# Optimization experiments

Measured on AMD Instinct MI355X. Metric: run time of the kernel, lower is better.

## Reference

```python
import jax, jax.numpy as jnp
import numpy as np

EMBED_DIM = 1024
NUM_HEADS = 16
DIM_K = EMBED_DIM // NUM_HEADS
B, S = 2, 2048


def setup_inputs() -> dict:
    key = jax.random.key(0)
    ks = jax.random.split(key, 7)
    scale = 1.0 / np.sqrt(EMBED_DIM)
    return {
        "query": jax.random.normal(ks[0], (B, S, EMBED_DIM), dtype=jnp.float32),
        "key": jax.random.normal(ks[1], (B, S, EMBED_DIM), dtype=jnp.float32),
        "value": jax.random.normal(ks[2], (B, S, EMBED_DIM), dtype=jnp.float32),
        "Wq": jax.random.normal(ks[3], (EMBED_DIM, EMBED_DIM), dtype=jnp.float32) * scale,
        "Wk": jax.random.normal(ks[4], (EMBED_DIM, EMBED_DIM), dtype=jnp.float32) * scale,
        "Wv": jax.random.normal(ks[5], (EMBED_DIM, EMBED_DIM), dtype=jnp.float32) * scale,
        "Wo": jax.random.normal(ks[6], (EMBED_DIM, EMBED_DIM), dtype=jnp.float32) * scale,
    }


def reference(query, key, value, Wq, Wk, Wv, Wo):
    b, s, e = query.shape
    # nn.Linear: y = x @ W.T  (bias=False)
    def proj(x, W):
        y = x @ W.T  # [b, s, e]
        return y.reshape(b, -1, NUM_HEADS, DIM_K).transpose(0, 2, 1, 3)  # [b, h, s, dk]

    q = proj(query, Wq)
    k = proj(key, Wk)
    v = proj(value, Wv)

    # attention: scores = q k^T / sqrt(dk); softmax; @ v  (dropout p=0 in eval)
    scores = jnp.einsum("bhqd,bhkd->bhqk", q, k) / jnp.sqrt(jnp.float32(DIM_K))
    attn = jax.nn.softmax(scores, axis=-1)
    x = jnp.einsum("bhqk,bhkd->bhqd", attn, v)  # [b, h, s, dk]

    x = x.transpose(0, 2, 1, 3).reshape(b, -1, e)  # merge heads
    return x @ Wo.T
```

## Files before the change

kernel.cpp:

```cpp
#include <hip/hip_runtime.h>
#include <hip/hip_bf16.h>
#include <stdint.h>

#define EMBED 1024
#define NHEAD 16
#define DKD   64
#define BATCH 2
#define SEQ   2048
#define MROWS (BATCH*SEQ)

typedef __attribute__((ext_vector_type(8)))  short bf16x8;
typedef __attribute__((ext_vector_type(4)))  float f32x4;
typedef __attribute__((ext_vector_type(16))) float f32x16;
typedef unsigned short u16;
typedef unsigned int   u32;
typedef __attribute__((ext_vector_type(4))) u32 u32x4;

__device__ inline u16 f2bf(float f) {
  return __builtin_bit_cast(u16, __float2bfloat16(f));
}

__device__ inline u32 cvtpk(float lo, float hi) {
  u32 r;
  asm("v_cvt_pk_bf16_f32 %0, %1, %2" : "=v"(r) : "v"(lo), "v"(hi));
  return r;
}

__device__ inline void plswap(u32& x, u32& y) {
  asm volatile("v_permlane32_swap_b32 %0, %1" : "+v"(x), "+v"(y));
}

__device__ inline void gload_lds16(const u16* g, u16* l) {
  __builtin_amdgcn_global_load_lds(
      (const __attribute__((address_space(1))) u32*)(const void*)g,
      (__attribute__((address_space(3))) u32*)(void*)l, 16, 0, 0);
}

__global__ __launch_bounds__(256) void cast_all(
    const float* __restrict__ s0, const float* __restrict__ s1,
    const float* __restrict__ s2, const float* __restrict__ s3,
    const float* __restrict__ s4, const float* __restrict__ s5,
    const float* __restrict__ s6,
    u16* __restrict__ d0, u16* __restrict__ d1, u16* __restrict__ d2,
    u16* __restrict__ d3, u16* __restrict__ d4, u16* __restrict__ d5,
    u16* __restrict__ d6) {
  const int y = blockIdx.y;
  const float* s; u16* d; int n4;
  switch (y) {
    case 0: s = s0; d = d0; n4 = MROWS*EMBED/4; break;
    case 1: s = s1; d = d1; n4 = MROWS*EMBED/4; break;
    case 2: s = s2; d = d2; n4 = MROWS*EMBED/4; break;
    case 3: s = s3; d = d3; n4 = EMBED*EMBED/4; break;
    case 4: s = s4; d = d4; n4 = EMBED*EMBED/4; break;
    case 5: s = s5; d = d5; n4 = EMBED*EMBED/4; break;
    default: s = s6; d = d6; n4 = EMBED*EMBED/4; break;
  }
  int i = blockIdx.x * 256 + threadIdx.x;
  int stride = gridDim.x * 256;
  for (int idx = i; idx < n4; idx += stride) {
    float4 f = ((const float4*)s)[idx];
    ushort4 o;
    o.x = f2bf(f.x); o.y = f2bf(f.y); o.z = f2bf(f.z); o.w = f2bf(f.w);
    ((ushort4*)d)[idx] = o;
  }
}

__global__ __launch_bounds__(256)
void gemm_qkv(const u16* __restrict__ A0, const u16* __restrict__ A1,
              const u16* __restrict__ A2, const u16* __restrict__ B0,
              const u16* __restrict__ B1, const u16* __restrict__ B2,
              u16* __restrict__ C0, u16* __restrict__ C1, u16* __restrict__ C2) {
  constexpr int K = EMBED;
  __shared__ u16 As[128 * 32];
  __shared__ u16 Bs[128 * 32];
  const int z = blockIdx.z;
  const u16* A = (z == 0) ? A0 : (z == 1) ? A1 : A2;
  const u16* B = (z == 0) ? B0 : (z == 1) ? B1 : B2;
  u16* C       = (z == 0) ? C0 : (z == 1) ? C1 : C2;

  const int t = threadIdx.x;
  const int w = t >> 6, l = t & 63;
  const int lr = l & 15, lg = l >> 4;
  const int m0 = blockIdx.x * 128;
  const int n0 = blockIdx.y * 128;
  const int wr = (w >> 1) * 64, wc = (w & 1) * 64;

  f32x4 acc[4][4] = {};

  const int srow = t >> 2;
  const int scol = (t & 3) * 8;
  const u16* Ag = A + (size_t)(m0 + srow) * K + scol;
  const u16* Bg = B + (size_t)(n0 + srow) * K + scol;
  u16* AsW = As + w * 512;
  u16* BsW = Bs + w * 512;
  const size_t rowstep = (size_t)64 * K;

  for (int k0 = 0; k0 < K; k0 += 32) {
    gload_lds16(Ag + k0,           AsW);
    gload_lds16(Ag + k0 + rowstep, AsW + 64 * 32);
    gload_lds16(Bg + k0,           BsW);
    gload_lds16(Bg + k0 + rowstep, BsW + 64 * 32);
    __syncthreads();
    bf16x8 a[4], b[4];
#pragma unroll
    for (int r = 0; r < 4; r++)
      a[r] = *(const bf16x8*)(As + (wr + r * 16 + lr) * 32 + 8 * lg);
#pragma unroll
    for (int c = 0; c < 4; c++)
      b[c] = *(const bf16x8*)(Bs + (wc + c * 16 + lr) * 32 + 8 * lg);
#pragma unroll
    for (int r = 0; r < 4; r++)
#pragma unroll
      for (int c = 0; c < 4; c++)
        acc[r][c] = __builtin_amdgcn_mfma_f32_16x16x32_bf16(a[r], b[c], acc[r][c], 0, 0, 0);
    __syncthreads();
  }

#pragma unroll
  for (int r = 0; r < 4; r++)
#pragma unroll
    for (int c = 0; c < 4; c++)
#pragma unroll
      for (int j = 0; j < 4; j++) {
        int m = m0 + wr + r * 16 + lg * 4 + j;
        int n = n0 + wc + c * 16 + lr;
        int b_ = m >> 11, s_ = m & 2047;
        int h_ = n >> 6,  d_ = n & 63;
        u16 vv = f2bf(acc[r][c][j]);
        if (z == 2)
          C[((size_t)(b_ * NHEAD + h_) * DKD + d_) * SEQ + s_] = vv;
        else
          C[(((size_t)(b_ * NHEAD + h_) * SEQ + s_) << 6) + d_] = vv;
      }
}

__global__ __launch_bounds__(256)
void gemm_out(const u16* __restrict__ A, const u16* __restrict__ B,
              float* __restrict__ C) {
  constexpr int K = EMBED, N = EMBED;
  __shared__ u16 As[64 * 32];
  __shared__ u16 Bs[128 * 32];
  const int t = threadIdx.x;
  const int w = t >> 6, l = t & 63;
  const int lr = l & 15, lg = l >> 4;
  const int m0 = blockIdx.x * 64;
  const int n0 = blockIdx.y * 128;
  const int wr = (w >> 1) * 32, wc = (w & 1) * 64;

  f32x4 acc[2][4] = {};

  const int srow = t >> 2;
  const int scol = (t & 3) * 8;
  const u16* Ag = A + (size_t)(m0 + srow) * K + scol;
  const u16* Bg = B + (size_t)(n0 + srow) * K + scol;
  u16* AsW = As + w * 512;
  u16* BsW = Bs + w * 512;
  const size_t rowstep = (size_t)64 * K;

  for (int k0 = 0; k0 < K; k0 += 32) {
    gload_lds16(Ag + k0,           AsW);
    gload_lds16(Bg + k0,           BsW);
    gload_lds16(Bg + k0 + rowstep, BsW + 64 * 32);
    __syncthreads();
    bf16x8 a[2], b[4];
#pragma unroll
    for (int r = 0; r < 2; r++)
      a[r] = *(const bf16x8*)(As + (wr + r * 16 + lr) * 32 + 8 * lg);
#pragma unroll
    for (int c = 0; c < 4; c++)
      b[c] = *(const bf16x8*)(Bs + (wc + c * 16 + lr) * 32 + 8 * lg);
#pragma unroll
    for (int r = 0; r < 2; r++)
#pragma unroll
      for (int c = 0; c < 4; c++)
        acc[r][c] = __builtin_amdgcn_mfma_f32_16x16x32_bf16(a[r], b[c], acc[r][c], 0, 0, 0);
    __syncthreads();
  }

#pragma unroll
  for (int r = 0; r < 2; r++)
#pragma unroll
    for (int c = 0; c < 4; c++)
#pragma unroll
      for (int j = 0; j < 4; j++) {
        int m = m0 + wr + r * 16 + lg * 4 + j;
        int n = n0 + wc + c * 16 + lr;
        C[(size_t)m * N + n] = acc[r][c][j];
      }
}

__global__ __launch_bounds__(256, 2)
void attn_kernel(const u16* __restrict__ Qh, const u16* __restrict__ Kh,
                 const u16* __restrict__ Vt, u16* __restrict__ Xo) {
  __shared__ u16 KV[2][8192];
  const int t = threadIdx.x, w = t >> 6, l = t & 63;
  const int q32 = l & 31, h = l >> 5;
  const int xcd = blockIdx.x & 7;
  const int li  = blockIdx.x >> 3;
  const int bh  = xcd * 4 + (li >> 4);
  const int qblk = li & 15;
  const int b_ = bh >> 4, h_ = bh & 15;
  const size_t base = (size_t)bh * SEQ * DKD;
  const u16* Kb = Kh + base;
  const u16* Vb = Vt + base;
  constexpr int NT = SEQ / 64;
  constexpr float C2 = 0.18033688f;
  constexpr float THR = 44.0f;

  const int qrow = qblk * 128 + w * 32 + q32;
  bf16x8 qf[4];
#pragma unroll
  for (int ks = 0; ks < 4; ks++)
    qf[ks] = *(const bf16x8*)(Qh + base + (size_t)qrow * DKD + ks * 16 + h * 8);

  f32x16 acc[2] = {};
  float m2 = -1e30f, lsum = 0.f;

  auto stage = [&](int buf, int kt) {
    u16* kd = &KV[buf][0];
    u16* vd = &KV[buf][4096];
    const int rb = w * 8 + (l >> 3);
    const int sg = (l & 7) ^ (l >> 3);
#pragma unroll
    for (int ch = 0; ch < 2; ch++) {
      int row = ch * 32 + rb;
      gload_lds16(Kb + (size_t)(kt * 64 + row) * DKD + sg * 8,
                  kd + (ch * 32 + w * 8) * 64);
      gload_lds16(Vb + (size_t)row * SEQ + kt * 64 + sg * 8,
                  vd + (ch * 32 + w * 8) * 64);
    }
  };

  auto compute = [&](int buf) {
    const u16* kd = &KV[buf][0];
    const u16* vd = &KV[buf][4096];
    f32x16 s[2] = {};
#pragma unroll
    for (int c = 0; c < 2; c++) {
      int row = c * 32 + q32;
#pragma unroll
      for (int ks = 0; ks < 4; ks++) {
        bf16x8 kf = *(const bf16x8*)(kd + row * 64 + (((2 * ks + h) ^ (row & 7)) * 8));
        s[c] = __builtin_amdgcn_mfma_f32_32x32x16_bf16(kf, qf[ks], s[c], 0, 0, 0);
      }
    }
    bf16x8 vf[2][4];
#pragma unroll
    for (int dc = 0; dc < 2; dc++) {
      int row = dc * 32 + q32;
#pragma unroll
      for (int tile = 0; tile < 4; tile++)
        vf[dc][tile] = *(const bf16x8*)(vd + row * 64 + (((2 * tile + h) ^ (row & 7)) * 8));
    }
    float pm = s[0][0];
#pragma unroll
    for (int r = 1; r < 16; r++) pm = fmaxf(pm, s[0][r]);
#pragma unroll
    for (int r = 0; r < 16; r++) pm = fmaxf(pm, s[1][r]);
    if (__any(pm > m2 + THR)) {
      float pmo = __shfl_xor(pm, 32, 64);
      float mn = fmaxf(m2, fmaxf(pm, pmo));
      float al = __builtin_amdgcn_exp2f((m2 - mn) * C2);
      lsum *= al;
#pragma unroll
      for (int dc = 0; dc < 2; dc++)
#pragma unroll
        for (int r = 0; r < 16; r++) acc[dc][r] *= al;
      m2 = mn;
    }
    const float nm = -m2 * C2;
    bf16x8 pfrag[4];
    float ls = 0.f;
#pragma unroll
    for (int c = 0; c < 2; c++) {
      float p[16];
#pragma unroll
      for (int r = 0; r < 16; r++) {
        p[r] = __builtin_amdgcn_exp2f(__builtin_fmaf(s[c][r], C2, nm));
        ls += p[r];
      }
      u32 Pk[8];
#pragma unroll
      for (int i = 0; i < 8; i++) Pk[i] = cvtpk(p[2 * i], p[2 * i + 1]);
      plswap(Pk[0], Pk[2]); plswap(Pk[1], Pk[3]);
      plswap(Pk[4], Pk[6]); plswap(Pk[5], Pk[7]);
      pfrag[2 * c]     = __builtin_bit_cast(bf16x8, (u32x4){Pk[0], Pk[1], Pk[2], Pk[3]});
      pfrag[2 * c + 1] = __builtin_bit_cast(bf16x8, (u32x4){Pk[4], Pk[5], Pk[6], Pk[7]});
    }
    lsum += ls;
#pragma unroll
    for (int tile = 0; tile < 4; tile++)
#pragma unroll
      for (int dc = 0; dc < 2; dc++)
        acc[dc] = __builtin_amdgcn_mfma_f32_32x32x16_bf16(vf[dc][tile], pfrag[tile], acc[dc], 0, 0, 0);
  };

  stage(0, 0);
  __syncthreads();
  int cur = 0;
  for (int kt = 0; kt < NT; kt++) {
    if (kt + 1 < NT) stage(cur ^ 1, kt + 1);
    compute(cur);
    __syncthreads();
    cur ^= 1;
  }

  lsum += __shfl_xor(lsum, 32, 64);
  float inv = 1.0f / lsum;
  u16* orow = Xo + ((size_t)b_ * SEQ + qrow) * EMBED + h_ * DKD;
#pragma unroll
  for (int dc = 0; dc < 2; dc++)
#pragma unroll
    for (int k4 = 0; k4 < 4; k4++) {
      u32 w0 = cvtpk(acc[dc][4 * k4 + 0] * inv, acc[dc][4 * k4 + 1] * inv);
      u32 w1 = cvtpk(acc[dc][4 * k4 + 2] * inv, acc[dc][4 * k4 + 3] * inv);
      int d = dc * 32 + k4 * 8 + h * 4;
      uint2 pk; pk.x = w0; pk.y = w1;
      *(uint2*)(orow + d) = pk;
    }
}

extern "C" void kernel_launch(void* const* d_in, const int* in_sizes, int n_in,
                              void* d_out, int out_size, void* d_ws, size_t ws_size,
                              hipStream_t stream) {
  const float* q  = (const float*)d_in[0];
  const float* k  = (const float*)d_in[1];
  const float* v  = (const float*)d_in[2];
  const float* Wq = (const float*)d_in[3];
  const float* Wk = (const float*)d_in[4];
  const float* Wv = (const float*)d_in[5];
  const float* Wo = (const float*)d_in[6];

  char* ws = (char*)d_ws;
  const size_t SZ_X = (size_t)MROWS * EMBED * 2;
  const size_t SZ_W = (size_t)EMBED * EMBED * 2;
  u16* qbf  = (u16*)(ws);
  u16* kbf  = (u16*)(ws + SZ_X);
  u16* vbf  = (u16*)(ws + 2 * SZ_X);
  u16* wqb  = (u16*)(ws + 3 * SZ_X);
  u16* wkb  = (u16*)(ws + 3 * SZ_X + SZ_W);
  u16* wvb  = (u16*)(ws + 3 * SZ_X + 2 * SZ_W);
  u16* wob  = (u16*)(ws + 3 * SZ_X + 3 * SZ_W);
  u16* Qh   = (u16*)(ws + 3 * SZ_X + 4 * SZ_W);
  u16* Kh   = (u16*)(ws + 4 * SZ_X + 4 * SZ_W);
  u16* Vt   = (u16*)(ws + 5 * SZ_X + 4 * SZ_W);
  u16* Xcat = (u16*)(ws + 6 * SZ_X + 4 * SZ_W);

  cast_all<<<dim3(1024, 7), 256, 0, stream>>>(q, k, v, Wq, Wk, Wv, Wo,
                                              qbf, kbf, vbf, wqb, wkb, wvb, wob);

  gemm_qkv<<<dim3(MROWS / 128, EMBED / 128, 3), 256, 0, stream>>>(
      qbf, kbf, vbf, wqb, wkb, wvb, Qh, Kh, Vt);

  attn_kernel<<<512, 256, 0, stream>>>(Qh, Kh, Vt, Xcat);

  gemm_out<<<dim3(MROWS / 64, EMBED / 128), 256, 0, stream>>>(Xcat, wob, (float*)d_out);
}
```

Before: 122.4 us.

## Split attention KV range across two wave groups and merge partial softmax

Doubles the attention block to 512 threads; two groups of four waves each process half the key sequence for the same 128 query rows with separate LDS double buffers. After the loop, the second half's partial accumulators, max and sum are written to LDS and merged by the first half with rescaling before output. It also changes the LDS swizzle to include the chunk and wave index, and turns the row-max and row-sum reductions into trees for more ILP. The aim is more waves per CU and shorter serial KV loops to hide latency, in exchange for higher LDS use, an extra merge step and fewer blocks resident per CU.

```diff
diff --git a/kernel.cpp b/kernel.cpp
--- a/kernel.cpp
+++ b/kernel.cpp
@@ -189,12 +189,13 @@
       }
 }
 
-__global__ __launch_bounds__(256, 2)
+__global__ __launch_bounds__(512, 4)
 void attn_kernel(const u16* __restrict__ Qh, const u16* __restrict__ Kh,
                  const u16* __restrict__ Vt, u16* __restrict__ Xo) {
-  __shared__ u16 KV[2][8192];
+  __shared__ u16 KV[2][2][8192];
   const int t = threadIdx.x, w = t >> 6, l = t & 63;
   const int q32 = l & 31, h = l >> 5;
+  const int hv = w >> 2, wq = w & 3;
   const int xcd = blockIdx.x & 7;
   const int li  = blockIdx.x >> 3;
   const int bh  = xcd * 4 + (li >> 4);
@@ -203,11 +204,11 @@
   const size_t base = (size_t)bh * SEQ * DKD;
   const u16* Kb = Kh + base;
   const u16* Vb = Vt + base;
-  constexpr int NT = SEQ / 64;
+  constexpr int NT2 = SEQ / 64 / 2;
   constexpr float C2 = 0.18033688f;
   constexpr float THR = 44.0f;
 
-  const int qrow = qblk * 128 + w * 32 + q32;
+  const int qrow = qblk * 128 + wq * 32 + q32;
   bf16x8 qf[4];
 #pragma unroll
   for (int ks = 0; ks < 4; ks++)
@@ -217,30 +218,32 @@
   float m2 = -1e30f, lsum = 0.f;
 
   auto stage = [&](int buf, int kt) {
-    u16* kd = &KV[buf][0];
-    u16* vd = &KV[buf][4096];
-    const int rb = w * 8 + (l >> 3);
-    const int sg = (l & 7) ^ (l >> 3);
+    u16* kd = &KV[hv][buf][0];
+    u16* vd = &KV[hv][buf][4096];
+    const int rb = wq * 8 + (l >> 3);
+    const int ktile = hv * NT2 + kt;
 #pragma unroll
     for (int ch = 0; ch < 2; ch++) {
       int row = ch * 32 + rb;
-      gload_lds16(Kb + (size_t)(kt * 64 + row) * DKD + sg * 8,
-                  kd + (ch * 32 + w * 8) * 64);
-      gload_lds16(Vb + (size_t)row * SEQ + kt * 64 + sg * 8,
-                  vd + (ch * 32 + w * 8) * 64);
+      int sg = (l & 7) ^ (l >> 3) ^ (ch * 4 + wq);
+      gload_lds16(Kb + (size_t)(ktile * 64 + row) * DKD + sg * 8,
+                  kd + (ch * 32 + wq * 8) * 64);
+      gload_lds16(Vb + (size_t)row * SEQ + ktile * 64 + sg * 8,
+                  vd + (ch * 32 + wq * 8) * 64);
     }
   };
 
   auto compute = [&](int buf) {
-    const u16* kd = &KV[buf][0];
-    const u16* vd = &KV[buf][4096];
+    const u16* kd = &KV[hv][buf][0];
+    const u16* vd = &KV[hv][buf][4096];
     f32x16 s[2] = {};
 #pragma unroll
     for (int c = 0; c < 2; c++) {
       int row = c * 32 + q32;
+      int key = (q32 & 7) ^ (c * 4 + (q32 >> 3));
 #pragma unroll
       for (int ks = 0; ks < 4; ks++) {
-        bf16x8 kf = *(const bf16x8*)(kd + row * 64 + (((2 * ks + h) ^ (row & 7)) * 8));
+        bf16x8 kf = *(const bf16x8*)(kd + row * 64 + (((2 * ks + h) ^ key) * 8));
         s[c] = __builtin_amdgcn_mfma_f32_32x32x16_bf16(kf, qf[ks], s[c], 0, 0, 0);
       }
     }
@@ -248,15 +251,19 @@
 #pragma unroll
     for (int dc = 0; dc < 2; dc++) {
       int row = dc * 32 + q32;
+      int key = (q32 & 7) ^ (dc * 4 + (q32 >> 3));
 #pragma unroll
       for (int tile = 0; tile < 4; tile++)
-        vf[dc][tile] = *(const bf16x8*)(vd + row * 64 + (((2 * tile + h) ^ (row & 7)) * 8));
-    }
-    float pm = s[0][0];
-#pragma unroll
-    for (int r = 1; r < 16; r++) pm = fmaxf(pm, s[0][r]);
-#pragma unroll
-    for (int r = 0; r < 16; r++) pm = fmaxf(pm, s[1][r]);
+        vf[dc][tile] = *(const bf16x8*)(vd + row * 64 + (((2 * tile + h) ^ key) * 8));
+    }
+    float mx[16];
+#pragma unroll
+    for (int r = 0; r < 16; r++) mx[r] = fmaxf(s[0][r], s[1][r]);
+#pragma unroll
+    for (int off = 8; off >= 1; off >>= 1)
+#pragma unroll
+      for (int r = 0; r < off; r++) mx[r] = fmaxf(mx[r], mx[r + off]);
+    float pm = mx[0];
     if (__any(pm > m2 + THR)) {
       float pmo = __shfl_xor(pm, 32, 64);
       float mn = fmaxf(m2, fmaxf(pm, pmo));
@@ -275,10 +282,11 @@
     for (int c = 0; c < 2; c++) {
       float p[16];
 #pragma unroll
-      for (int r = 0; r < 16; r++) {
+      for (int r = 0; r < 16; r++)
         p[r] = __builtin_amdgcn_exp2f(__builtin_fmaf(s[c][r], C2, nm));
-        ls += p[r];
-      }
+      float s0 = ((p[0] + p[1]) + (p[2] + p[3])) + ((p[4] + p[5]) + (p[6] + p[7]));
+      float s1 = ((p[8] + p[9]) + (p[10] + p[11])) + ((p[12] + p[13]) + (p[14] + p[15]));
+      ls += s0 + s1;
       u32 Pk[8];
 #pragma unroll
       for (int i = 0; i < 8; i++) Pk[i] = cvtpk(p[2 * i], p[2 * i + 1]);
@@ -298,26 +306,51 @@
   stage(0, 0);
   __syncthreads();
   int cur = 0;
-  for (int kt = 0; kt < NT; kt++) {
-    if (kt + 1 < NT) stage(cur ^ 1, kt + 1);
+  for (int kt = 0; kt < NT2; kt++) {
+    if (kt + 1 < NT2) stage(cur ^ 1, kt + 1);
     compute(cur);
     __syncthreads();
     cur ^= 1;
   }
 
-  lsum += __shfl_xor(lsum, 32, 64);
-  float inv = 1.0f / lsum;
-  u16* orow = Xo + ((size_t)b_ * SEQ + qrow) * EMBED + h_ * DKD;
-#pragma unroll
-  for (int dc = 0; dc < 2; dc++)
-#pragma unroll
-    for (int k4 = 0; k4 < 4; k4++) {
-      u32 w0 = cvtpk(acc[dc][4 * k4 + 0] * inv, acc[dc][4 * k4 + 1] * inv);
-      u32 w1 = cvtpk(acc[dc][4 * k4 + 2] * inv, acc[dc][4 * k4 + 3] * inv);
-      int d = dc * 32 + k4 * 8 + h * 4;
-      uint2 pk; pk.x = w0; pk.y = w1;
-      *(uint2*)(orow + d) = pk;
-    }
+  float* shf = (float*)&KV[0][0][0];
+  if (hv == 1) {
+    float* dst = shf + (size_t)(wq * 64 + l) * 36;
+#pragma unroll
+    for (int dc = 0; dc < 2; dc++)
+#pragma unroll
+      for (int k4 = 0; k4 < 4; k4++) {
+        float4 v4o = {acc[dc][4 * k4 + 0], acc[dc][4 * k4 + 1],
+                      acc[dc][4 * k4 + 2], acc[dc][4 * k4 + 3]};
+        *(float4*)(dst + dc * 16 + k4 * 4) = v4o;
+      }
+    dst[32] = m2;
+    dst[33] = lsum;
+  }
+  __syncthreads();
+  if (hv == 0) {
+    const float* src = shf + (size_t)(wq * 64 + l) * 36;
+    float m2b = src[32], lsb = src[33];
+    float mN = fmaxf(m2, m2b);
+    float a0 = __builtin_amdgcn_exp2f((m2 - mN) * C2);
+    float a1 = __builtin_amdgcn_exp2f((m2b - mN) * C2);
+    float lv = lsum * a0 + lsb * a1;
+    lv += __shfl_xor(lv, 32, 64);
+    float inv = 1.0f / lv;
+    u16* orow = Xo + ((size_t)b_ * SEQ + qrow) * EMBED + h_ * DKD;
+#pragma unroll
+    for (int dc = 0; dc < 2; dc++)
+#pragma unroll
+      for (int k4 = 0; k4 < 4; k4++) {
+        float4 ob = *(const float4*)(src + dc * 16 + k4 * 4);
+        float o0 = (acc[dc][4 * k4 + 0] * a0 + ob.x * a1) * inv;
+        float o1 = (acc[dc][4 * k4 + 1] * a0 + ob.y * a1) * inv;
+        float o2 = (acc[dc][4 * k4 + 2] * a0 + ob.z * a1) * inv;
+        float o3 = (acc[dc][4 * k4 + 3] * a0 + ob.w * a1) * inv;
+        uint2 pk; pk.x = cvtpk(o0, o1); pk.y = cvtpk(o2, o3);
+        *(uint2*)(orow + dc * 32 + k4 * 8 + h * 4) = pk;
+      }
+  }
 }
 
 extern "C" void kernel_launch(void* const* d_in, const int* in_sizes, int n_in,
@@ -352,7 +385,7 @@
   gemm_qkv<<<dim3(MROWS / 128, EMBED / 128, 3), 256, 0, stream>>>(
       qbf, kbf, vbf, wqb, wkb, wvb, Qh, Kh, Vt);
 
-  attn_kernel<<<512, 256, 0, stream>>>(Qh, Kh, Vt, Xcat);
+  attn_kernel<<<512, 512, 0, stream>>>(Qh, Kh, Vt, Xcat);
 
   gemm_out<<<dim3(MROWS / 64, EMBED / 128), 256, 0, stream>>>(Xcat, wob, (float*)d_out);
 }
```

New measurement: 146.8 us. 20.0% more time.

## Split attention over key halves with a separate log-sum-exp combine kernel

Applied to the files above, without the earlier changes.

Splits the attention key sequence into two halves, doubling the grid to 1024 blocks. Each block writes partial normalized outputs plus per-row max and sum, and a new combine kernel merges the two halves with log-sum-exp weights. Launch bounds are raised to four blocks per SM. The goal is better occupancy and CU fill on the MI355X's many CUs for the 512-block attention. The cost is an extra kernel launch, extra global traffic for the partials, and an extra bf16 rounding of the partial outputs.

```diff
diff --git a/kernel.cpp b/kernel.cpp
--- a/kernel.cpp
+++ b/kernel.cpp
@@ -18,6 +18,10 @@
 
 __device__ inline u16 f2bf(float f) {
   return __builtin_bit_cast(u16, __float2bfloat16(f));
+}
+__device__ inline float bf2f(u16 x) {
+  u32 u = ((u32)x) << 16;
+  return __builtin_bit_cast(float, u);
 }
 
 __device__ inline u32 cvtpk(float lo, float hi) {
@@ -189,9 +193,10 @@
       }
 }
 
-__global__ __launch_bounds__(256, 2)
-void attn_kernel(const u16* __restrict__ Qh, const u16* __restrict__ Kh,
-                 const u16* __restrict__ Vt, u16* __restrict__ Xo) {
+__global__ __launch_bounds__(256, 4)
+void attn_part(const u16* __restrict__ Qh, const u16* __restrict__ Kh,
+               const u16* __restrict__ Vt, u16* __restrict__ Opart,
+               float* __restrict__ MLpart) {
   __shared__ u16 KV[2][8192];
   const int t = threadIdx.x, w = t >> 6, l = t & 63;
   const int q32 = l & 31, h = l >> 5;
@@ -199,11 +204,11 @@
   const int li  = blockIdx.x >> 3;
   const int bh  = xcd * 4 + (li >> 4);
   const int qblk = li & 15;
-  const int b_ = bh >> 4, h_ = bh & 15;
+  const int hv = blockIdx.y;
   const size_t base = (size_t)bh * SEQ * DKD;
   const u16* Kb = Kh + base;
   const u16* Vb = Vt + base;
-  constexpr int NT = SEQ / 64;
+  constexpr int NT2 = SEQ / 64 / 2;
   constexpr float C2 = 0.18033688f;
   constexpr float THR = 44.0f;
 
@@ -221,12 +226,13 @@
     u16* vd = &KV[buf][4096];
     const int rb = w * 8 + (l >> 3);
     const int sg = (l & 7) ^ (l >> 3);
+    const int ktile = hv * NT2 + kt;
 #pragma unroll
     for (int ch = 0; ch < 2; ch++) {
       int row = ch * 32 + rb;
-      gload_lds16(Kb + (size_t)(kt * 64 + row) * DKD + sg * 8,
+      gload_lds16(Kb + (size_t)(ktile * 64 + row) * DKD + sg * 8,
                   kd + (ch * 32 + w * 8) * 64);
-      gload_lds16(Vb + (size_t)row * SEQ + kt * 64 + sg * 8,
+      gload_lds16(Vb + (size_t)row * SEQ + ktile * 64 + sg * 8,
                   vd + (ch * 32 + w * 8) * 64);
     }
   };
@@ -298,26 +304,61 @@
   stage(0, 0);
   __syncthreads();
   int cur = 0;
-  for (int kt = 0; kt < NT; kt++) {
-    if (kt + 1 < NT) stage(cur ^ 1, kt + 1);
+  for (int kt = 0; kt < NT2; kt++) {
+    if (kt + 1 < NT2) stage(cur ^ 1, kt + 1);
     compute(cur);
     __syncthreads();
     cur ^= 1;
   }
 
-  lsum += __shfl_xor(lsum, 32, 64);
-  float inv = 1.0f / lsum;
-  u16* orow = Xo + ((size_t)b_ * SEQ + qrow) * EMBED + h_ * DKD;
+  const float lpair = lsum + __shfl_xor(lsum, 32, 64);
+  const float invl = 1.0f / lpair;
+  const int entry = (bh * 16 + qblk) * 2 + hv;
+  u16* op = Opart + (size_t)entry * (128 * 64) + (size_t)(w * 32 + q32) * 64;
 #pragma unroll
   for (int dc = 0; dc < 2; dc++)
 #pragma unroll
     for (int k4 = 0; k4 < 4; k4++) {
-      u32 w0 = cvtpk(acc[dc][4 * k4 + 0] * inv, acc[dc][4 * k4 + 1] * inv);
-      u32 w1 = cvtpk(acc[dc][4 * k4 + 2] * inv, acc[dc][4 * k4 + 3] * inv);
-      int d = dc * 32 + k4 * 8 + h * 4;
-      uint2 pk; pk.x = w0; pk.y = w1;
-      *(uint2*)(orow + d) = pk;
-    }
+      uint2 pk;
+      pk.x = cvtpk(acc[dc][4 * k4 + 0] * invl, acc[dc][4 * k4 + 1] * invl);
+      pk.y = cvtpk(acc[dc][4 * k4 + 2] * invl, acc[dc][4 * k4 + 3] * invl);
+      *(uint2*)(op + dc * 32 + k4 * 8 + h * 4) = pk;
+    }
+  if (h == 0) {
+    float2 ml; ml.x = m2; ml.y = lpair;
+    *(float2*)(MLpart + (size_t)entry * 256 + (w * 32 + q32) * 2) = ml;
+  }
+}
+
+__global__ __launch_bounds__(256)
+void attn_combine(const u16* __restrict__ Opart, const float* __restrict__ MLpart,
+                  u16* __restrict__ Xo) {
+  constexpr float C2 = 0.18033688f;
+  int tid = blockIdx.x * 256 + threadIdx.x;
+  int d8 = tid & 7;
+  int qq = (tid >> 3) & 2047;
+  int bh = tid >> 14;
+  int qblk = qq >> 7, qi = qq & 127;
+  int e0 = (bh * 16 + qblk) * 2;
+  float2 ml0 = *(const float2*)(MLpart + (size_t)e0 * 256 + qi * 2);
+  float2 ml1 = *(const float2*)(MLpart + (size_t)(e0 + 1) * 256 + qi * 2);
+  float mN = fmaxf(ml0.x, ml1.x);
+  float w0 = __builtin_amdgcn_exp2f((ml0.x - mN) * C2) * ml0.y;
+  float w1 = __builtin_amdgcn_exp2f((ml1.x - mN) * C2) * ml1.y;
+  float inv = 1.0f / (w0 + w1);
+  w0 *= inv; w1 *= inv;
+  bf16x8 o0 = *(const bf16x8*)(Opart + (size_t)e0 * 8192 + qi * 64 + d8 * 8);
+  bf16x8 o1 = *(const bf16x8*)(Opart + (size_t)(e0 + 1) * 8192 + qi * 64 + d8 * 8);
+  u32 ow[4];
+#pragma unroll
+  for (int i = 0; i < 4; i++) {
+    float f0 = bf2f((u16)o0[2 * i])     * w0 + bf2f((u16)o1[2 * i])     * w1;
+    float f1 = bf2f((u16)o0[2 * i + 1]) * w0 + bf2f((u16)o1[2 * i + 1]) * w1;
+    ow[i] = cvtpk(f0, f1);
+  }
+  int b_ = bh >> 4, h_ = bh & 15;
+  *(u32x4*)(Xo + ((size_t)b_ * SEQ + qq) * EMBED + h_ * DKD + d8 * 8) =
+      (u32x4){ow[0], ow[1], ow[2], ow[3]};
 }
 
 extern "C" void kernel_launch(void* const* d_in, const int* in_sizes, int n_in,
@@ -346,13 +387,17 @@
   u16* Vt   = (u16*)(ws + 5 * SZ_X + 4 * SZ_W);
   u16* Xcat = (u16*)(ws + 6 * SZ_X + 4 * SZ_W);
 
+  u16*   Opart  = (u16*)(ws);
+  float* MLpart = (float*)(ws + 2 * SZ_X);
+
   cast_all<<<dim3(1024, 7), 256, 0, stream>>>(q, k, v, Wq, Wk, Wv, Wo,
                                               qbf, kbf, vbf, wqb, wkb, wvb, wob);
 
   gemm_qkv<<<dim3(MROWS / 128, EMBED / 128, 3), 256, 0, stream>>>(
       qbf, kbf, vbf, wqb, wkb, wvb, Qh, Kh, Vt);
 
-  attn_kernel<<<512, 256, 0, stream>>>(Qh, Kh, Vt, Xcat);
+  attn_part<<<dim3(512, 2), 256, 0, stream>>>(Qh, Kh, Vt, Opart, MLpart);
+  attn_combine<<<2048, 256, 0, stream>>>(Opart, MLpart, Xcat);
 
   gemm_out<<<dim3(MROWS / 64, EMBED / 128), 256, 0, stream>>>(Xcat, wob, (float*)d_out);
 }
```

Result: slower. 137.3 us (+12.2%).

## Double-buffer LDS in projection GEMMs and raise wave priority around attention MFMAs

Applied to the files above, without the earlier changes.

Both projection GEMMs now keep two LDS buffers and issue the next K-slice's global-to-LDS loads before computing on the current slice. This overlaps memory latency with MFMA work and drops one barrier per iteration. The attention kernel also wraps its QK and PV MFMA blocks in s_setprio so those waves get scheduling priority over others on the CU. The cost is doubled LDS use in the GEMMs, which may lower occupancy, and a possible race, since the prefetch load is issued without an explicit wait before the barrier.

```diff
diff --git a/kernel.cpp b/kernel.cpp
--- a/kernel.cpp
+++ b/kernel.cpp
@@ -71,8 +71,8 @@
               const u16* __restrict__ B1, const u16* __restrict__ B2,
               u16* __restrict__ C0, u16* __restrict__ C1, u16* __restrict__ C2) {
   constexpr int K = EMBED;
-  __shared__ u16 As[128 * 32];
-  __shared__ u16 Bs[128 * 32];
+  __shared__ u16 As[2][128 * 32];
+  __shared__ u16 Bs[2][128 * 32];
   const int z = blockIdx.z;
   const u16* A = (z == 0) ? A0 : (z == 1) ? A1 : A2;
   const u16* B = (z == 0) ? B0 : (z == 1) ? B1 : B2;
@@ -91,29 +91,34 @@
   const int scol = (t & 3) * 8;
   const u16* Ag = A + (size_t)(m0 + srow) * K + scol;
   const u16* Bg = B + (size_t)(n0 + srow) * K + scol;
-  u16* AsW = As + w * 512;
-  u16* BsW = Bs + w * 512;
   const size_t rowstep = (size_t)64 * K;
 
+  auto stage = [&](int buf, int k0) {
+    gload_lds16(Ag + k0,           As[buf] + w * 512);
+    gload_lds16(Ag + k0 + rowstep, As[buf] + 64 * 32 + w * 512);
+    gload_lds16(Bg + k0,           Bs[buf] + w * 512);
+    gload_lds16(Bg + k0 + rowstep, Bs[buf] + 64 * 32 + w * 512);
+  };
+
+  stage(0, 0);
+  __syncthreads();
+  int cur = 0;
   for (int k0 = 0; k0 < K; k0 += 32) {
-    gload_lds16(Ag + k0,           AsW);
-    gload_lds16(Ag + k0 + rowstep, AsW + 64 * 32);
-    gload_lds16(Bg + k0,           BsW);
-    gload_lds16(Bg + k0 + rowstep, BsW + 64 * 32);
-    __syncthreads();
+    if (k0 + 32 < K) stage(cur ^ 1, k0 + 32);
     bf16x8 a[4], b[4];
 #pragma unroll
     for (int r = 0; r < 4; r++)
-      a[r] = *(const bf16x8*)(As + (wr + r * 16 + lr) * 32 + 8 * lg);
+      a[r] = *(const bf16x8*)(As[cur] + (wr + r * 16 + lr) * 32 + 8 * lg);
 #pragma unroll
     for (int c = 0; c < 4; c++)
-      b[c] = *(const bf16x8*)(Bs + (wc + c * 16 + lr) * 32 + 8 * lg);
+      b[c] = *(const bf16x8*)(Bs[cur] + (wc + c * 16 + lr) * 32 + 8 * lg);
 #pragma unroll
     for (int r = 0; r < 4; r++)
 #pragma unroll
       for (int c = 0; c < 4; c++)
         acc[r][c] = __builtin_amdgcn_mfma_f32_16x16x32_bf16(a[r], b[c], acc[r][c], 0, 0, 0);
     __syncthreads();
+    cur ^= 1;
   }
 
 #pragma unroll
@@ -138,8 +143,8 @@
 void gemm_out(const u16* __restrict__ A, const u16* __restrict__ B,
               float* __restrict__ C) {
   constexpr int K = EMBED, N = EMBED;
-  __shared__ u16 As[64 * 32];
-  __shared__ u16 Bs[128 * 32];
+  __shared__ u16 As[2][64 * 32];
+  __shared__ u16 Bs[2][128 * 32];
   const int t = threadIdx.x;
   const int w = t >> 6, l = t & 63;
   const int lr = l & 15, lg = l >> 4;
@@ -153,28 +158,33 @@
   const int scol = (t & 3) * 8;
   const u16* Ag = A + (size_t)(m0 + srow) * K + scol;
   const u16* Bg = B + (size_t)(n0 + srow) * K + scol;
-  u16* AsW = As + w * 512;
-  u16* BsW = Bs + w * 512;
   const size_t rowstep = (size_t)64 * K;
 
+  auto stage = [&](int buf, int k0) {
+    gload_lds16(Ag + k0,           As[buf] + w * 512);
+    gload_lds16(Bg + k0,           Bs[buf] + w * 512);
+    gload_lds16(Bg + k0 + rowstep, Bs[buf] + 64 * 32 + w * 512);
+  };
+
+  stage(0, 0);
+  __syncthreads();
+  int cur = 0;
   for (int k0 = 0; k0 < K; k0 += 32) {
-    gload_lds16(Ag + k0,           AsW);
-    gload_lds16(Bg + k0,           BsW);
-    gload_lds16(Bg + k0 + rowstep, BsW + 64 * 32);
-    __syncthreads();
+    if (k0 + 32 < K) stage(cur ^ 1, k0 + 32);
     bf16x8 a[2], b[4];
 #pragma unroll
     for (int r = 0; r < 2; r++)
-      a[r] = *(const bf16x8*)(As + (wr + r * 16 + lr) * 32 + 8 * lg);
+      a[r] = *(const bf16x8*)(As[cur] + (wr + r * 16 + lr) * 32 + 8 * lg);
 #pragma unroll
     for (int c = 0; c < 4; c++)
-      b[c] = *(const bf16x8*)(Bs + (wc + c * 16 + lr) * 32 + 8 * lg);
+      b[c] = *(const bf16x8*)(Bs[cur] + (wc + c * 16 + lr) * 32 + 8 * lg);
 #pragma unroll
     for (int r = 0; r < 2; r++)
 #pragma unroll
       for (int c = 0; c < 4; c++)
         acc[r][c] = __builtin_amdgcn_mfma_f32_16x16x32_bf16(a[r], b[c], acc[r][c], 0, 0, 0);
     __syncthreads();
+    cur ^= 1;
   }
 
 #pragma unroll
@@ -235,6 +245,7 @@
     const u16* kd = &KV[buf][0];
     const u16* vd = &KV[buf][4096];
     f32x16 s[2] = {};
+    __builtin_amdgcn_s_setprio(1);
 #pragma unroll
     for (int c = 0; c < 2; c++) {
       int row = c * 32 + q32;
@@ -244,6 +255,7 @@
         s[c] = __builtin_amdgcn_mfma_f32_32x32x16_bf16(kf, qf[ks], s[c], 0, 0, 0);
       }
     }
+    __builtin_amdgcn_s_setprio(0);
     bf16x8 vf[2][4];
 #pragma unroll
     for (int dc = 0; dc < 2; dc++) {
@@ -288,11 +300,13 @@
       pfrag[2 * c + 1] = __builtin_bit_cast(bf16x8, (u32x4){Pk[4], Pk[5], Pk[6], Pk[7]});
     }
     lsum += ls;
+    __builtin_amdgcn_s_setprio(1);
 #pragma unroll
     for (int tile = 0; tile < 4; tile++)
 #pragma unroll
       for (int dc = 0; dc < 2; dc++)
         acc[dc] = __builtin_amdgcn_mfma_f32_32x32x16_bf16(vf[dc][tile], pfrag[tile], acc[dc], 0, 0, 0);
+    __builtin_amdgcn_s_setprio(0);
   };
 
   stage(0, 0);
```

New measurement: 132.5 us. 1.08x slower.
